# Performance work log

Measured on AMD Instinct MI355X. Metric: run time of the kernel, lower is better.

The kernel has to match this reference:

```python
import jax, jax.numpy as jnp
import numpy as np

B, H, S = 16, 1024, 2048

def setup_inputs() -> dict:
    key = jax.random.key(0)
    kf, kz, ki = jax.random.split(key, 3)
    f = jax.random.uniform(kf, (B, H, S), dtype=jnp.float32)
    z = jax.random.normal(kz, (B, H, S), dtype=jnp.float32)
    i = jax.random.uniform(ki, (B, H, S), dtype=jnp.float32)
    return {"f": f, "z": z, "i": i}

def reference(f, z, i):
    # Inputs are [batch, hidden, seq]; recurrence runs over seq:
    #   h_t = f_t * h_{t-1} + i_t * z_t, h_{-1} = 0
    fs = jnp.transpose(f, (2, 0, 1))  # [S, B, H]
    xs = jnp.transpose(i * z, (2, 0, 1))  # [S, B, H]

    def step(h_prev, fx):
        f_t, x_t = fx
        h_t = f_t * h_prev + x_t
        return h_t, h_t

    h0 = jnp.zeros(fs.shape[1:], dtype=fs.dtype)
    _, hs = jax.lax.scan(step, h0, (fs, xs))  # [S, B, H]
    return jnp.transpose(hs, (1, 2, 0))  # [B, H, S]
```

## Files before the change

### kernel.cpp

```cpp
#include <hip/hip_runtime.h>


constexpr int S_LEN = 2048;
constexpr int TPB   = 512;

__global__ __launch_bounds__(TPB) void ifo_scan_kernel(
    const float* __restrict__ f,
    const float* __restrict__ z,
    const float* __restrict__ iin,
    float* __restrict__ out)
{
    const size_t base = (size_t)blockIdx.x * S_LEN;
    const int t    = threadIdx.x;
    const int lane = t & 63;
    const int wave = t >> 6;

    const float4 ff = reinterpret_cast<const float4*>(f   + base)[t];
    const float4 zz = reinterpret_cast<const float4*>(z   + base)[t];
    const float4 ii = reinterpret_cast<const float4*>(iin + base)[t];

    float4 xx;
    xx.x = ii.x * zz.x;
    xx.y = ii.y * zz.y;
    xx.z = ii.z * zz.z;
    xx.w = ii.w * zz.w;

    float A = ff.x, B = xx.x;
    A = ff.y * A;  B = ff.y * B + xx.y;
    A = ff.z * A;  B = ff.z * B + xx.z;
    A = ff.w * A;  B = ff.w * B + xx.w;

    float a = A, b = B;
    #pragma unroll
    for (int d = 1; d < 64; d <<= 1) {
        float a_up = __shfl_up(a, d);
        float b_up = __shfl_up(b, d);
        if (lane >= d) {
            b = a * b_up + b;
            a = a * a_up;
        }
    }

    __shared__ float wa[8], wb[8];
    if (lane == 63) { wa[wave] = a; wb[wave] = b; }
    __syncthreads();

    float pa = 1.0f, pb = 0.0f;
    for (int w = 0; w < wave; ++w) {
        pb = wa[w] * pb + wb[w];
        pa = wa[w] * pa;
    }

    float ea = __shfl_up(a, 1);
    float eb = __shfl_up(b, 1);
    if (lane == 0) { ea = 1.0f; eb = 0.0f; }

    float h = ea * pb + eb;
    (void)pa;

    float4 oo;
    h = ff.x * h + xx.x;  oo.x = h;
    h = ff.y * h + xx.y;  oo.y = h;
    h = ff.z * h + xx.z;  oo.z = h;
    h = ff.w * h + xx.w;  oo.w = h;
    reinterpret_cast<float4*>(out + base)[t] = oo;
}

extern "C" void kernel_launch(void* const* d_in, const int* in_sizes, int n_in,
                              void* d_out, int out_size, void* d_ws, size_t ws_size,
                              hipStream_t stream) {
    const float* f = (const float*)d_in[0];
    const float* z = (const float*)d_in[1];
    const float* i = (const float*)d_in[2];
    float* out = (float*)d_out;

    const int rows = out_size / S_LEN;
    ifo_scan_kernel<<<rows, TPB, 0, stream>>>(f, z, i, out);
}
```

Before: 384.6 us.

## Assign one wave per row with serial chunk carry instead of block-wide scan

Each wavefront now processes a whole 2048-element row as eight 256-element chunks, running a wave-level shuffle scan per chunk and chaining chunks through a scalar carry. This removes the shared-memory cross-wave combine and __syncthreads, and packs four independent rows per block. In exchange each thread holds many more registers (eight float4 pairs) and does eight sequential shuffle scans, which may reduce occupancy and lengthen the per-wave critical path.

```diff
diff --git a/kernel.cpp b/kernel.cpp
--- a/kernel.cpp
+++ b/kernel.cpp
@@ -1,69 +1,85 @@
 #include <hip/hip_runtime.h>
 
 
-constexpr int S_LEN = 2048;
-constexpr int TPB   = 512;
+constexpr int S_LEN  = 2048;
+constexpr int WAVES  = 4;
+constexpr int TPB    = 64 * WAVES;
+constexpr int K_SUB  = S_LEN / 256;
 
 __global__ __launch_bounds__(TPB) void ifo_scan_kernel(
     const float* __restrict__ f,
     const float* __restrict__ z,
     const float* __restrict__ iin,
-    float* __restrict__ out)
+    float* __restrict__ out,
+    int n_rows)
 {
-    const size_t base = (size_t)blockIdx.x * S_LEN;
-    const int t    = threadIdx.x;
-    const int lane = t & 63;
-    const int wave = t >> 6;
+    const int lane = threadIdx.x & 63;
+    const int wv   = threadIdx.x >> 6;
+    const size_t row = (size_t)blockIdx.x * WAVES + wv;
+    if (row >= (size_t)n_rows) return;
+    const size_t base = row * S_LEN;
 
-    const float4 ff = reinterpret_cast<const float4*>(f   + base)[t];
-    const float4 zz = reinterpret_cast<const float4*>(z   + base)[t];
-    const float4 ii = reinterpret_cast<const float4*>(iin + base)[t];
+    const float4* __restrict__ F = reinterpret_cast<const float4*>(f   + base);
+    const float4* __restrict__ Z = reinterpret_cast<const float4*>(z   + base);
+    const float4* __restrict__ I = reinterpret_cast<const float4*>(iin + base);
+    float4* __restrict__ O = reinterpret_cast<float4*>(out + base);
 
-    float4 xx;
-    xx.x = ii.x * zz.x;
-    xx.y = ii.y * zz.y;
-    xx.z = ii.z * zz.z;
-    xx.w = ii.w * zz.w;
+    float4 ff[K_SUB], xx[K_SUB];
+    #pragma unroll
+    for (int k = 0; k < K_SUB; ++k) {
+        ff[k] = F[k * 64 + lane];
+        const float4 zz = Z[k * 64 + lane];
+        const float4 ii = I[k * 64 + lane];
+        xx[k].x = ii.x * zz.x;
+        xx[k].y = ii.y * zz.y;
+        xx[k].z = ii.z * zz.z;
+        xx[k].w = ii.w * zz.w;
+    }
 
-    float A = ff.x, B = xx.x;
-    A = ff.y * A;  B = ff.y * B + xx.y;
-    A = ff.z * A;  B = ff.z * B + xx.z;
-    A = ff.w * A;  B = ff.w * B + xx.w;
+    float a[K_SUB], b[K_SUB];
+    #pragma unroll
+    for (int k = 0; k < K_SUB; ++k) {
+        float A = ff[k].x, B = xx[k].x;
+        A = ff[k].y * A;  B = ff[k].y * B + xx[k].y;
+        A = ff[k].z * A;  B = ff[k].z * B + xx[k].z;
+        A = ff[k].w * A;  B = ff[k].w * B + xx[k].w;
+        a[k] = A; b[k] = B;
+    }
 
-    float a = A, b = B;
     #pragma unroll
-    for (int d = 1; d < 64; d <<= 1) {
-        float a_up = __shfl_up(a, d);
-        float b_up = __shfl_up(b, d);
-        if (lane >= d) {
-            b = a * b_up + b;
-            a = a * a_up;
+    for (int k = 0; k < K_SUB; ++k) {
+        #pragma unroll
+        for (int d = 1; d < 64; d <<= 1) {
+            float a_up = __shfl_up(a[k], d);
+            float b_up = __shfl_up(b[k], d);
+            if (lane >= d) {
+                b[k] = a[k] * b_up + b[k];
+                a[k] = a[k] * a_up;
+            }
         }
     }
 
-    __shared__ float wa[8], wb[8];
-    if (lane == 63) { wa[wave] = a; wb[wave] = b; }
-    __syncthreads();
+    float h_carry = 0.0f;
+    #pragma unroll
+    for (int k = 0; k < K_SUB; ++k) {
+        float ea = __shfl_up(a[k], 1);
+        float eb = __shfl_up(b[k], 1);
+        if (lane == 0) { ea = 1.0f; eb = 0.0f; }
+        float h = ea * h_carry + eb;
 
-    float pa = 1.0f, pb = 0.0f;
-    for (int w = 0; w < wave; ++w) {
-        pb = wa[w] * pb + wb[w];
-        pa = wa[w] * pa;
+        const float ta = __shfl(a[k], 63);
+        const float tb = __shfl(b[k], 63);
+        const float next = ta * h_carry + tb;
+
+        float4 oo;
+        h = ff[k].x * h + xx[k].x;  oo.x = h;
+        h = ff[k].y * h + xx[k].y;  oo.y = h;
+        h = ff[k].z * h + xx[k].z;  oo.z = h;
+        h = ff[k].w * h + xx[k].w;  oo.w = h;
+        O[k * 64 + lane] = oo;
+
+        h_carry = next;
     }
-
-    float ea = __shfl_up(a, 1);
-    float eb = __shfl_up(b, 1);
-    if (lane == 0) { ea = 1.0f; eb = 0.0f; }
-
-    float h = ea * pb + eb;
-    (void)pa;
-
-    float4 oo;
-    h = ff.x * h + xx.x;  oo.x = h;
-    h = ff.y * h + xx.y;  oo.y = h;
-    h = ff.z * h + xx.z;  oo.z = h;
-    h = ff.w * h + xx.w;  oo.w = h;
-    reinterpret_cast<float4*>(out + base)[t] = oo;
 }
 
 extern "C" void kernel_launch(void* const* d_in, const int* in_sizes, int n_in,
@@ -75,5 +91,6 @@
     float* out = (float*)d_out;
 
     const int rows = out_size / S_LEN;
-    ifo_scan_kernel<<<rows, TPB, 0, stream>>>(f, z, i, out);
+    const int grid = (rows + WAVES - 1) / WAVES;
+    ifo_scan_kernel<<<grid, TPB, 0, stream>>>(f, z, i, out, rows);
 }
```

New measurement: 390.6 us. No clear change (+1.6%).
